# Optimization experiments

Measured on AMD Instinct MI355X. Metric: run time of the kernel, lower is better.

The kernel has to match this reference:

```python
import jax, jax.numpy as jnp
import numpy as np

# FlowNetC correlation hyperparameters (from init_kwargs)
PAD = 20
KS = 1
MD = 20
S1 = 1
S2 = 2
MUL = 1


def setup_inputs() -> dict:
    key = jax.random.key(0)
    k1, k2 = jax.random.split(key)
    B, C, H, W = 8, 256, 96, 128
    input1 = jax.random.normal(k1, (B, C, H, W), dtype=jnp.float32)
    input2 = jax.random.normal(k2, (B, C, H, W), dtype=jnp.float32)
    return {"input1": input1, "input2": input2}


def _correlation(in1, in2):
    b, c, h, w = in1.shape
    p1 = jnp.pad(in1, ((0, 0), (0, 0), (PAD, PAD), (PAD, PAD)))
    p2 = jnp.pad(in2, ((0, 0), (0, 0), (PAD, PAD), (PAD, PAD)))
    hp, wp = h + 2 * PAD, w + 2 * PAD
    out_h = (hp - 2 * MD - KS) // S1 + 1
    out_w = (wp - 2 * MD - KS) // S1 + 1
    d = 2 * MD // S2 + 1  # number of displacement steps per axis (21)

    # fixed center region of input1: [b, c, out_h, out_w]
    region1 = p1[:, :, MD:MD + out_h * S1:S1, MD:MD + out_w * S1:S1]

    offs = (jnp.arange(d) - d // 2) * S2  # displacement offsets
    dys, dxs = jnp.meshgrid(offs, offs, indexing='ij')
    dys = dys.reshape(-1)
    dxs = dxs.reshape(-1)

    def step(carry, dydx):
        dy, dx = dydx
        y0 = MD + dy
        x0 = MD + dx
        valid = (y0 >= 0) & (x0 >= 0) & (y0 + out_h * S1 <= hp) & (x0 + out_w * S1 <= wp)
        reg2 = jax.lax.dynamic_slice(
            p2, (0, 0, y0, x0), (b, c, out_h * S1, out_w * S1)
        )[:, :, ::S1, ::S1]
        corr = (region1 * reg2).sum(axis=1) * MUL  # [b, out_h, out_w]
        corr = jnp.where(valid, corr, jnp.zeros_like(corr))
        return carry, corr

    _, chans = jax.lax.scan(step, None, (dys, dxs))  # [d*d, b, out_h, out_w]
    return jnp.transpose(chans, (1, 0, 2, 3))  # [b, d*d, out_h, out_w]


def reference(input1, input2):
    return _correlation(input1, input2)
```

## Files before the change

kernel.cpp:

```cpp
#include <hip/hip_runtime.h>
#include <stdint.h>

#define B_N   8
#define C_N   256
#define H_N   96
#define W_N   128
#define NCK   8
#define ND    21
#define NK    (ND * ND)

typedef __attribute__((ext_vector_type(8))) short short8;
typedef __attribute__((ext_vector_type(4))) float f32x4;

__device__ char zchunk[12288];

__device__ __forceinline__ uint32_t f2bf(float f) {
  uint32_t u = __builtin_bit_cast(uint32_t, f);
  return (u + 0x7fffu + ((u >> 16) & 1u)) >> 16;
}
__device__ __forceinline__ uint32_t packbf(float lo, float hi) {
  return f2bf(lo) | (f2bf(hi) << 16);
}

__global__ __launch_bounds__(256) void prep(const float* __restrict__ in1,
                                            const float* __restrict__ in2,
                                            unsigned short* __restrict__ Apre,
                                            unsigned short* __restrict__ Bpre) {
  __shared__ float tile[32][W_N + 1];
  int blk = blockIdx.x;
  bool isA = blk < 6144;
  int rblk = isA ? blk : blk - 6144;
  int ck = rblk & 7, bi = rblk >> 3;
  int b = bi / H_N, row = bi % H_N;
  const float* src = (isA ? in1 : in2) + ((size_t)(b * C_N + ck * 32) * H_N + row) * W_N;
  int tid = threadIdx.x;
  for (int idx = tid; idx < 32 * W_N; idx += 256) {
    int c = idx >> 7, j = idx & 127;
    tile[c][j] = src[(size_t)c * (H_N * W_N) + j];
  }
  __syncthreads();
  if (isA) {
    uint32_t* dst = (uint32_t*)Apre + (size_t)rblk * 2048;
    for (int q = tid; q < 2048; q += 256) {
      int e2 = q & 3, ln = (q >> 2) & 63, tp = q >> 8;
      int t = tp >> 1, p = tp & 1;
      int m = ln & 15, kg = ln >> 4;
      int c0 = kg * 8 + 2 * e2;
      int j = 32 * t + 2 * m + p;
      dst[q] = packbf(tile[c0][j], tile[c0 + 1][j]);
    }
  } else {
    uint32_t* dst = (uint32_t*)Bpre + (size_t)rblk * 3072;
    for (int q = tid; q < 3072; q += 256) {
      int e2 = q & 3, ln = (q >> 2) & 63, sp = q >> 8;
      int s = sp >> 1, p = sp & 1;
      int m = ln & 15, kg = ln >> 4;
      int c0 = kg * 8 + 2 * e2;
      int x = 32 * s + 2 * m - 20 + p;
      dst[q] = ((unsigned)x < 128u) ? packbf(tile[c0][x], tile[c0 + 1][x]) : 0u;
    }
  }
}

__global__ __launch_bounds__(256, 3) void corr_main(const unsigned short* __restrict__ Apre,
                                                    const unsigned short* __restrict__ Bpre,
                                                    float* __restrict__ out) {
  __shared__ float outl[ND][W_N + 1];

  int h = blockIdx.x;
  int l = (h & 7) * 672 + (h >> 3);
  int bi = l / 7, gidx = l - 7 * bi;
  int b = bi / H_N, i = bi % H_N;
  int dyb = gidx * 3;

  int tid = threadIdx.x;
  int lane = tid & 63, w = tid >> 6;
  int p = w & 1, th = w >> 1;
  int m = lane & 15, kg = lane >> 4;

  f32x4 acc[2][3][3];
#pragma unroll
  for (int a0i = 0; a0i < 2; ++a0i)
#pragma unroll
    for (int a1i = 0; a1i < 3; ++a1i)
#pragma unroll
      for (int a2i = 0; a2i < 3; ++a2i) acc[a0i][a1i][a2i] = {0.f, 0.f, 0.f, 0.f};

  const char* Ap = (const char*)Apre + (size_t)bi * 65536
                   + (((4 * th + p)) << 10) + lane * 16;
  const char* Bp[3];
  int bstr[3];
#pragma unroll
  for (int g = 0; g < 3; ++g) {
    int y = i + 2 * (dyb + g) - 20;
    bool v = (unsigned)y < (unsigned)H_N;
    const char* base = v ? (const char*)Bpre + (size_t)(b * H_N + y) * 98304
                         : (const char*)zchunk;
    Bp[g] = base + ((4 * th + p) << 10) + lane * 16;
    bstr[g] = v ? 12288 : 0;
  }

#pragma unroll 2
  for (int ck = 0; ck < NCK; ++ck) {
    short8 a0 = *(const short8*)(Ap);
    short8 a1 = *(const short8*)(Ap + 2048);
    short8 bb[4][3];
#pragma unroll
    for (int ss = 0; ss < 4; ++ss)
#pragma unroll
      for (int g = 0; g < 3; ++g)
        bb[ss][g] = *(const short8*)(Bp[g] + ss * 2048);
#pragma unroll
    for (int ss = 0; ss < 4; ++ss)
#pragma unroll
      for (int g = 0; g < 3; ++g) {
        if (ss <= 2) acc[0][g][ss]     = __builtin_amdgcn_mfma_f32_16x16x32_bf16(a0, bb[ss][g], acc[0][g][ss], 0, 0, 0);
        if (ss >= 1) acc[1][g][ss - 1] = __builtin_amdgcn_mfma_f32_16x16x32_bf16(a1, bb[ss][g], acc[1][g][ss - 1], 0, 0, 0);
      }
    Ap += 8192;
    Bp[0] += bstr[0]; Bp[1] += bstr[1]; Bp[2] += bstr[2];
  }

#pragma unroll
  for (int g = 0; g < 3; ++g) {
    __syncthreads();
#pragma unroll
    for (int tt = 0; tt < 2; ++tt) {
      int t = 2 * th + tt;
#pragma unroll
      for (int dl = 0; dl < 3; ++dl) {
#pragma unroll
        for (int r = 0; r < 4; ++r) {
          int a_ = kg * 4 + r;
          int dxi = 16 * dl + m - a_;
          if (dxi >= 0 && dxi <= 20) {
            int j = 2 * (16 * t + a_) + p;
            outl[dxi][j] = acc[tt][g][dl][r];
          }
        }
      }
    }
    __syncthreads();
    int dyi = dyb + g;
    size_t obase = ((size_t)(b * NK + dyi * ND) * H_N + i) * W_N;
    for (int idx = tid; idx < ND * W_N; idx += 256) {
      int dxi = idx >> 7, j = idx & 127;
      out[obase + (size_t)dxi * (H_N * W_N) + j] = outl[dxi][j];
    }
  }
}

__global__ void corr_naive(const float* __restrict__ in1, const float* __restrict__ in2,
                           float* __restrict__ out) {
  size_t o = (size_t)blockIdx.x * 256 + threadIdx.x;
  const size_t total = (size_t)B_N * NK * H_N * W_N;
  if (o >= total) return;
  int j = o & 127;
  int i = (int)((o >> 7) % H_N);
  int k = (int)((o / ((size_t)H_N * W_N)) % NK);
  int b = (int)(o / ((size_t)NK * H_N * W_N));
  int dyi = k / ND, dxi = k % ND;
  int y = i + 2 * dyi - 20, x = j + 2 * dxi - 20;
  float s = 0.f;
  if ((unsigned)y < (unsigned)H_N && (unsigned)x < (unsigned)W_N) {
    const float* p1 = in1 + ((size_t)b * C_N * H_N + i) * W_N + j;
    const float* p2 = in2 + ((size_t)b * C_N * H_N + y) * W_N + x;
    for (int c = 0; c < C_N; ++c)
      s += p1[(size_t)c * H_N * W_N] * p2[(size_t)c * H_N * W_N];
  }
  out[o] = s;
}

extern "C" void kernel_launch(void* const* d_in, const int* in_sizes, int n_in,
                              void* d_out, int out_size, void* d_ws, size_t ws_size,
                              hipStream_t stream) {
  const float* in1 = (const float*)d_in[0];
  const float* in2 = (const float*)d_in[1];
  float* out = (float*)d_out;

  const size_t A_BYTES = (size_t)6144 * 8192;
  const size_t B_BYTES = (size_t)6144 * 12288;
  if (ws_size < A_BYTES + B_BYTES) {
    size_t total = (size_t)B_N * NK * H_N * W_N;
    corr_naive<<<(int)((total + 255) / 256), 256, 0, stream>>>(in1, in2, out);
    return;
  }
  unsigned short* Apre = (unsigned short*)d_ws;
  unsigned short* Bpre = (unsigned short*)((char*)d_ws + A_BYTES);

  prep<<<12288, 256, 0, stream>>>(in1, in2, Apre, Bpre);
  corr_main<<<5376, 256, 0, stream>>>(Apre, Bpre, out);
}
```

Measured before the change: 213.2 us.

## Share B rows across output rows via LDS with async double-buffered loads

Reorganizes corr_main so each 768-thread block is keyed by a source row Y of input2 and handles up to three output rows that all read the same three B rows. Those B rows are staged into LDS with global_load_lds async copies, double-buffered over channel chunks, instead of each wave reading B straight from global memory. The aim is to cut redundant global/L2 traffic for B. In exchange the grid mapping becomes irregular, some waves sit idle on edge rows, there is a barrier per chunk, and the LDS footprint grows to 72KB, which limits how many blocks fit per CU.

```diff
diff --git a/kernel.cpp b/kernel.cpp
--- a/kernel.cpp
+++ b/kernel.cpp
@@ -12,14 +12,17 @@
 typedef __attribute__((ext_vector_type(8))) short short8;
 typedef __attribute__((ext_vector_type(4))) float f32x4;
 
-__device__ char zchunk[12288];
-
 __device__ __forceinline__ uint32_t f2bf(float f) {
   uint32_t u = __builtin_bit_cast(uint32_t, f);
   return (u + 0x7fffu + ((u >> 16) & 1u)) >> 16;
 }
 __device__ __forceinline__ uint32_t packbf(float lo, float hi) {
   return f2bf(lo) | (f2bf(hi) << 16);
+}
+__device__ __forceinline__ void async16(void* lds_dst, const void* gsrc) {
+  __builtin_amdgcn_global_load_lds(
+      (const __attribute__((address_space(1))) void*)gsrc,
+      (__attribute__((address_space(3))) void*)lds_dst, 16, 0, 0);
 }
 
 __global__ __launch_bounds__(256) void prep(const float* __restrict__ in1,
@@ -62,22 +65,51 @@
   }
 }
 
-__global__ __launch_bounds__(256, 3) void corr_main(const unsigned short* __restrict__ Apre,
+__global__ __launch_bounds__(768, 3) void corr_main(const unsigned short* __restrict__ Apre,
                                                     const unsigned short* __restrict__ Bpre,
                                                     float* __restrict__ out) {
-  __shared__ float outl[ND][W_N + 1];
+  __shared__ __align__(16) char Bl[2][36864];
 
   int h = blockIdx.x;
-  int l = (h & 7) * 672 + (h >> 3);
-  int bi = l / 7, gidx = l - 7 * bi;
-  int b = bi / H_N, i = bi % H_N;
-  int dyb = gidx * 3;
+  int b = h & 7, blk = h >> 3;
+  int Y, pos;
+  if (blk < 18)       { Y = blk - 20;                pos = 0; }
+  else if (blk < 54)  { int t = blk - 18;  Y = -2 + (t >> 1); pos = t & 1; }
+  else if (blk < 234) { int t = blk - 54;  Y = 16 + t / 3;    pos = t % 3; }
+  else if (blk < 270) { int t = blk - 234; Y = 76 + (t >> 1); pos = t & 1; }
+  else                { Y = 94 + (blk - 270);        pos = 0; }
+  int g_min = (Y > 75) ? (Y - 70) / 6 : 0;
+  int g_max = (Y + 20) / 6; if (g_max > 6) g_max = 6;
 
   int tid = threadIdx.x;
   int lane = tid & 63, w = tid >> 6;
-  int p = w & 1, th = w >> 1;
+  int rr = w >> 2, sub = w & 3;
+  int p = sub & 1, th = sub >> 1;
   int m = lane & 15, kg = lane >> 4;
 
+  int gidx = g_min + pos * 3 + rr;
+  bool act = gidx <= g_max;
+  int i_el = Y + 20 - 6 * gidx;
+  int dyb = 3 * gidx;
+
+  const char* bsrc[3];
+  bool yval[3];
+#pragma unroll
+  for (int k = 0; k < 3; ++k) {
+    int y = Y + 2 * k;
+    yval[k] = (unsigned)y < (unsigned)H_N;
+    bsrc[k] = (const char*)Bpre + (size_t)((b * H_N + (yval[k] ? y : 0)) * NCK) * 12288
+              + w * 1024 + lane * 16;
+  }
+#pragma unroll
+  for (int k = 0; k < 3; ++k) {
+    if (!yval[k]) {
+      short8 z = {};
+      *(short8*)(&Bl[0][0] + k * 12288 + w * 1024 + lane * 16) = z;
+      *(short8*)(&Bl[1][0] + k * 12288 + w * 1024 + lane * 16) = z;
+    }
+  }
+
   f32x4 acc[2][3][3];
 #pragma unroll
   for (int a0i = 0; a0i < 2; ++a0i)
@@ -86,67 +118,72 @@
 #pragma unroll
       for (int a2i = 0; a2i < 3; ++a2i) acc[a0i][a1i][a2i] = {0.f, 0.f, 0.f, 0.f};
 
-  const char* Ap = (const char*)Apre + (size_t)bi * 65536
-                   + (((4 * th + p)) << 10) + lane * 16;
-  const char* Bp[3];
-  int bstr[3];
+  const char* Ap = (const char*)Apre + (size_t)(b * H_N + (act ? i_el : 0)) * 65536
+                   + ((4 * th + p) << 10) + lane * 16;
+
+#pragma unroll
+  for (int k = 0; k < 3; ++k)
+    if (yval[k]) async16(&Bl[0][0] + k * 12288 + w * 1024, bsrc[k]);
+  __syncthreads();
+
+  for (int ck = 0; ck < NCK; ++ck) {
+    char* cur = &Bl[ck & 1][0];
+    if (ck < NCK - 1) {
+      char* nxt = &Bl[(ck + 1) & 1][0];
+#pragma unroll
+      for (int k = 0; k < 3; ++k)
+        if (yval[k]) async16(nxt + k * 12288 + w * 1024, bsrc[k] + (size_t)(ck + 1) * 12288);
+    }
+    if (act) {
+      short8 a0 = *(const short8*)(Ap);
+      short8 a1 = *(const short8*)(Ap + 2048);
+#pragma unroll
+      for (int ss = 0; ss < 4; ++ss) {
+        int s = 2 * th + ss;
+#pragma unroll
+        for (int g = 0; g < 3; ++g) {
+          short8 bbv = *(const short8*)(cur + g * 12288 + ((2 * s + p) << 10) + lane * 16);
+          if (ss <= 2) acc[0][g][ss]     = __builtin_amdgcn_mfma_f32_16x16x32_bf16(a0, bbv, acc[0][g][ss], 0, 0, 0);
+          if (ss >= 1) acc[1][g][ss - 1] = __builtin_amdgcn_mfma_f32_16x16x32_bf16(a1, bbv, acc[1][g][ss - 1], 0, 0, 0);
+        }
+      }
+    }
+    Ap += 8192;
+    __syncthreads();
+  }
+
+  float* outl = (float*)(&Bl[0][0] + rr * 11072);
+  int gt = sub * 64 + lane;
 #pragma unroll
   for (int g = 0; g < 3; ++g) {
-    int y = i + 2 * (dyb + g) - 20;
-    bool v = (unsigned)y < (unsigned)H_N;
-    const char* base = v ? (const char*)Bpre + (size_t)(b * H_N + y) * 98304
-                         : (const char*)zchunk;
-    Bp[g] = base + ((4 * th + p) << 10) + lane * 16;
-    bstr[g] = v ? 12288 : 0;
-  }
-
-#pragma unroll 2
-  for (int ck = 0; ck < NCK; ++ck) {
-    short8 a0 = *(const short8*)(Ap);
-    short8 a1 = *(const short8*)(Ap + 2048);
-    short8 bb[4][3];
-#pragma unroll
-    for (int ss = 0; ss < 4; ++ss)
-#pragma unroll
-      for (int g = 0; g < 3; ++g)
-        bb[ss][g] = *(const short8*)(Bp[g] + ss * 2048);
-#pragma unroll
-    for (int ss = 0; ss < 4; ++ss)
-#pragma unroll
-      for (int g = 0; g < 3; ++g) {
-        if (ss <= 2) acc[0][g][ss]     = __builtin_amdgcn_mfma_f32_16x16x32_bf16(a0, bb[ss][g], acc[0][g][ss], 0, 0, 0);
-        if (ss >= 1) acc[1][g][ss - 1] = __builtin_amdgcn_mfma_f32_16x16x32_bf16(a1, bb[ss][g], acc[1][g][ss - 1], 0, 0, 0);
-      }
-    Ap += 8192;
-    Bp[0] += bstr[0]; Bp[1] += bstr[1]; Bp[2] += bstr[2];
-  }
-
-#pragma unroll
-  for (int g = 0; g < 3; ++g) {
-    __syncthreads();
-#pragma unroll
-    for (int tt = 0; tt < 2; ++tt) {
-      int t = 2 * th + tt;
-#pragma unroll
-      for (int dl = 0; dl < 3; ++dl) {
-#pragma unroll
-        for (int r = 0; r < 4; ++r) {
-          int a_ = kg * 4 + r;
-          int dxi = 16 * dl + m - a_;
-          if (dxi >= 0 && dxi <= 20) {
-            int j = 2 * (16 * t + a_) + p;
-            outl[dxi][j] = acc[tt][g][dl][r];
+    if (act) {
+#pragma unroll
+      for (int tt = 0; tt < 2; ++tt) {
+        int t = 2 * th + tt;
+#pragma unroll
+        for (int dl = 0; dl < 3; ++dl) {
+#pragma unroll
+          for (int r = 0; r < 4; ++r) {
+            int a_ = kg * 4 + r;
+            int dxi = 16 * dl + m - a_;
+            if (dxi >= 0 && dxi <= 20) {
+              int j = 2 * (16 * t + a_) + p;
+              outl[dxi * 129 + j] = acc[tt][g][dl][r];
+            }
           }
         }
       }
     }
     __syncthreads();
-    int dyi = dyb + g;
-    size_t obase = ((size_t)(b * NK + dyi * ND) * H_N + i) * W_N;
-    for (int idx = tid; idx < ND * W_N; idx += 256) {
-      int dxi = idx >> 7, j = idx & 127;
-      out[obase + (size_t)dxi * (H_N * W_N) + j] = outl[dxi][j];
-    }
+    if (act) {
+      int dyi = dyb + g;
+      size_t obase = ((size_t)(b * NK + dyi * ND) * H_N + i_el) * W_N;
+      for (int idx = gt; idx < ND * W_N; idx += 256) {
+        int dxi = idx >> 7, j = idx & 127;
+        out[obase + (size_t)dxi * (H_N * W_N) + j] = outl[dxi * 129 + j];
+      }
+    }
+    __syncthreads();
   }
 }
 
@@ -189,5 +226,5 @@
   unsigned short* Bpre = (unsigned short*)((char*)d_ws + A_BYTES);
 
   prep<<<12288, 256, 0, stream>>>(in1, in2, Apre, Bpre);
-  corr_main<<<5376, 256, 0, stream>>>(Apre, Bpre, out);
-}
+  corr_main<<<2304, 768, 0, stream>>>(Apre, Bpre, out);
+}
```

New measurement: 200.4 us. 1.06x faster.
